# Performance work log

Measured on AMD Instinct MI355X. Metric: run time of the kernel, lower is better.

## Reference

```python
import jax, jax.numpy as jnp
import numpy as np

N, D, H, E = 32768, 1024, 1024, 4


def setup_inputs() -> dict:
    key = jax.random.key(0)
    ks = jax.random.split(key, 10)
    s = 0.02  # xavier-ish init scale for stability
    return {
        "features": jax.random.normal(ks[0], (N, D), dtype=jnp.float32),
        "symbol_ids": jax.random.randint(ks[1], (N,), 0, E, dtype=jnp.int32),
        "W1": jax.random.normal(ks[2], (E, D, H), dtype=jnp.float32) * s,
        "b1": jax.random.normal(ks[3], (E, H), dtype=jnp.float32) * s,
        "W2": jax.random.normal(ks[4], (E, H, H), dtype=jnp.float32) * s,
        "b2": jax.random.normal(ks[5], (E, H), dtype=jnp.float32) * s,
        "W3": jax.random.normal(ks[6], (E, H, 1), dtype=jnp.float32) * s,
        "b3": jax.random.normal(ks[7], (E, 1), dtype=jnp.float32) * s,
        "slope": jax.random.normal(ks[8], (E,), dtype=jnp.float32),
        "intercept": jax.random.normal(ks[9], (E,), dtype=jnp.float32),
    }


def reference(features, symbol_ids, W1, b1, W2, b2, W3, b3, slope, intercept):
    # Run every atom through every expert MLP (E is tiny), then select by symbol.
    # h1: [E, N, H]
    h = jax.nn.relu(jnp.einsum("nd,edh->enh", features, W1) + b1[:, None, :])
    h = jax.nn.relu(jnp.einsum("enh,ehk->enk", h, W2) + b2[:, None, :])
    y = (jnp.einsum("enk,eko->eno", h, W3) + b3[:, None, :])[..., 0]  # [E, N]
    per_atom = slope[:, None] * y + intercept[:, None]                # [E, N]
    sel = symbol_ids[None, :] == jnp.arange(E, dtype=symbol_ids.dtype)[:, None]
    atomic_energies = jnp.sum(jnp.where(sel, per_atom, 0.0), axis=0)  # [N]
    image_energy = jnp.sum(atomic_energies)                           # scalar
    return image_energy
```

## Files before the change

kernel.cpp:

```cpp
#include <hip/hip_runtime.h>
#include <hip/hip_bf16.h>
#include <stdint.h>

#define NATOMS 32768
#define DDIM   1024
#define HDIM   1024
#define ENUM   4
#define MCAP   (NATOMS + ENUM * 128)
#define MTILES 260

typedef unsigned short u16;
typedef unsigned char  u8;
typedef __attribute__((ext_vector_type(8)))  int   i32x8;
typedef __attribute__((ext_vector_type(16))) float f32x16;

static const size_t XP_OFF   = 0;
static const size_t H1_OFF   = XP_OFF  + (size_t)MCAP * 1024;
static const size_t W1T_OFF  = H1_OFF  + (size_t)MCAP * 1024;
static const size_t W2T_OFF  = W1T_OFF + (size_t)ENUM * 1024 * 1024;
static const size_t PERM_OFF = W2T_OFF + (size_t)ENUM * 1024 * 1024;
static const size_t META_OFF = PERM_OFF + (size_t)MCAP * 4;

__device__ __forceinline__ u8 f2fp8(float x) {
    int w = __builtin_amdgcn_cvt_pk_fp8_f32(x, x, 0, false);
    return (u8)(w & 0xFF);
}

__global__ void k_count(const int* __restrict__ sym, int* __restrict__ meta) {
    __shared__ int cnt[4];
    int t = threadIdx.x;
    if (t < 4) cnt[t] = 0;
    __syncthreads();
    int n = blockIdx.x * 256 + t;
    int lane = t & 63;
    int e = sym[n];
#pragma unroll
    for (int j = 0; j < ENUM; ++j) {
        unsigned long long mask = __ballot(e == j);
        if (mask) {
            int leader = __ffsll((long long)mask) - 1;
            if (lane == leader) atomicAdd(&cnt[j], __popcll(mask));
        }
    }
    __syncthreads();
    if (t < 4) meta[256 + blockIdx.x * 4 + t] = cnt[t];
}

__global__ void k_offsets(int* __restrict__ meta, const float* __restrict__ slope,
                          const float* __restrict__ b3, const float* __restrict__ inter,
                          float* __restrict__ out) {
    __shared__ int tot[4];
    int t = threadIdx.x;
    if (t < 4) {
        int s = 0;
#pragma unroll 8
        for (int b = 0; b < 128; ++b) s += meta[256 + b * 4 + t];
        tot[t] = s;
    }
    __syncthreads();
    if (t == 0) {
        int off = 0;
        float c = 0.f;
        for (int e = 0; e < 4; ++e) {
            int cnt = tot[e];
            meta[e * 16]     = cnt;
            meta[128 + e]    = off;
            meta[64 + e*16]  = off;
            c += (float)cnt * (slope[e] * b3[e] + inter[e]);
            off += (cnt + 127) & ~127;
        }
        meta[132] = off;
        out[0] = c;
    }
}

__global__ void k_scatter(const int* __restrict__ sym, int* __restrict__ meta,
                          int* __restrict__ perm) {
    int n = blockIdx.x * 256 + threadIdx.x;
    int lane = threadIdx.x & 63;
    int e = sym[n];
#pragma unroll
    for (int j = 0; j < ENUM; ++j) {
        unsigned long long mask = __ballot(e == j);
        if (mask) {
            int leader = __ffsll((long long)mask) - 1;
            int base = 0;
            if (lane == leader)
                base = atomicAdd(&meta[64 + j * 16], __popcll(mask));
            base = __shfl(base, leader, 64);
            if (e == j) {
                int rank = __popcll(mask & ((1ull << lane) - 1ull));
                perm[base + rank] = n;
            }
        }
    }
}

__global__ void k_convx(const float* __restrict__ F, const int* __restrict__ perm,
                        const int* __restrict__ meta, u8* __restrict__ Xp) {
    int g = blockIdx.x * 256 + threadIdx.x;
    int slot = g >> 7, c = g & 127;
    const int* offs = meta + 128;
    int e = (slot >= offs[1]) + (slot >= offs[2]) + (slot >= offs[3]);
    bool valid = slot < offs[e] + meta[e * 16];
    uint2 v;
    if (!valid) {
        v.x = 0u; v.y = 0u;
    } else {
        int src = perm[slot];
        const float* fp = F + (size_t)src * 1024 + c * 8;
        int w0 = 0, w1 = 0;
        w0 = __builtin_amdgcn_cvt_pk_fp8_f32(fp[0], fp[1], w0, false);
        w0 = __builtin_amdgcn_cvt_pk_fp8_f32(fp[2], fp[3], w0, true);
        w1 = __builtin_amdgcn_cvt_pk_fp8_f32(fp[4], fp[5], w1, false);
        w1 = __builtin_amdgcn_cvt_pk_fp8_f32(fp[6], fp[7], w1, true);
        v.x = (unsigned)w0; v.y = (unsigned)w1;
    }
    *(uint2*)(void*)(Xp + (size_t)g * 8) = v;
}

__global__ void k_transw(const float* __restrict__ W1, u8* __restrict__ W1T,
                         const float* __restrict__ W2, u8* __restrict__ W2T) {
    __shared__ u8 tile[64][65];
    const float* W  = blockIdx.z ? W2  : W1;
    u8*          WT = blockIdx.z ? W2T : W1T;
    int e  = blockIdx.y;
    int tn = blockIdx.x & 15;
    int tk = blockIdx.x >> 4;
    const float* Wp = W  + (size_t)e * 1024 * 1024;
    u8*         WTp = WT + (size_t)e * 1024 * 1024;
    int c = threadIdx.x & 63, r0 = threadIdx.x >> 6;
#pragma unroll
    for (int i = 0; i < 16; ++i) {
        int r = r0 + i * 4;
        tile[r][c] = f2fp8(32.0f * Wp[(size_t)(tk * 64 + r) * 1024 + tn * 64 + c]);
    }
    __syncthreads();
#pragma unroll
    for (int i = 0; i < 16; ++i) {
        int r = r0 + i * 4;
        WTp[(size_t)(tn * 64 + r) * 1024 + tk * 64 + c] = tile[c][r];
    }
}

template <bool FUSE>
__global__ __launch_bounds__(256, 4)
void k_gemm(const u8* __restrict__ A, const u8* __restrict__ BT,
            const float* __restrict__ bias, u8* __restrict__ C,
            const int* __restrict__ meta, const float* __restrict__ W3,
            const float* __restrict__ slope, float* __restrict__ out) {
    __shared__ u8 As[128 * 128];
    __shared__ u8 Bs[128 * 128];
    const int* offs = meta + 128;

    const int flat = blockIdx.y * 8 + blockIdx.x;
    const int mt = (flat >> 6) * 8 + (flat & 7);
    const int nt = (flat & 63) >> 3;
    if (mt >= MTILES) return;
    const int m0 = mt * 128, n0 = nt * 128;
    int e = (m0 >= offs[1]) + (m0 >= offs[2]) + (m0 >= offs[3]);

    const int t = threadIdx.x;
    const int w = t >> 6, lane = t & 63;
    const int l31 = lane & 31, khalf = lane >> 5;
    const int wm = w & 1, wn = w >> 1;

    const u8* Ag = A + (size_t)m0 * 1024;
    const u8* Bg = BT + (size_t)e * 1024 * 1024 + (size_t)n0 * 1024;

    const int srow   = t >> 3;
    const int gchunk = (t & 7) ^ (srow & 7);

    f32x16 acc[2][2] = {};

    for (int kt = 0; kt < 1024 / 128; ++kt) {
        const int kb = kt * 128;
#pragma unroll
        for (int i = 0; i < 4; ++i) {
            int row = i * 32 + srow;
            __builtin_amdgcn_global_load_lds(
                (const void*)(Ag + (size_t)row * 1024 + kb + gchunk * 16),
                (void*)(As + i * 4096 + w * 1024), 16, 0, 0);
        }
#pragma unroll
        for (int i = 0; i < 4; ++i) {
            int row = i * 32 + srow;
            __builtin_amdgcn_global_load_lds(
                (const void*)(Bg + (size_t)row * 1024 + kb + gchunk * 16),
                (void*)(Bs + i * 4096 + w * 1024), 16, 0, 0);
        }
        __syncthreads();

#pragma unroll
        for (int kk = 0; kk < 2; ++kk) {
            const int c0 = 4 * kk + 2 * khalf;
            i32x8 a[2], b[2];
#pragma unroll
            for (int mi = 0; mi < 2; ++mi) {
                int m = wm * 64 + mi * 32 + l31;
                const u8* base = As + m * 128;
                int lo = ((c0 ^ (m & 7)) << 4);
                uint4 q0 = *(const uint4*)(const void*)(base + lo);
                uint4 q1 = *(const uint4*)(const void*)(base + (lo ^ 16));
                union { uint4 q[2]; i32x8 v; } u;
                u.q[0] = q0; u.q[1] = q1;
                a[mi] = u.v;
            }
#pragma unroll
            for (int ni = 0; ni < 2; ++ni) {
                int n = wn * 64 + ni * 32 + l31;
                const u8* base = Bs + n * 128;
                int lo = ((c0 ^ (n & 7)) << 4);
                uint4 q0 = *(const uint4*)(const void*)(base + lo);
                uint4 q1 = *(const uint4*)(const void*)(base + (lo ^ 16));
                union { uint4 q[2]; i32x8 v; } u;
                u.q[0] = q0; u.q[1] = q1;
                b[ni] = u.v;
            }
#pragma unroll
            for (int mi = 0; mi < 2; ++mi)
#pragma unroll
                for (int ni = 0; ni < 2; ++ni)
                    acc[mi][ni] = __builtin_amdgcn_mfma_scale_f32_32x32x64_f8f6f4(
                        a[mi], b[ni], acc[mi][ni],
                        0, 0,
                        0, 0x7F7F7F7F,
                        0, 0x7A7A7A7A);
        }
        __syncthreads();
    }

    if (!FUSE) {
#pragma unroll
        for (int ni = 0; ni < 2; ++ni) {
            int col = n0 + wn * 64 + ni * 32 + l31;
            float bv = bias[e * 1024 + col];
#pragma unroll
            for (int mi = 0; mi < 2; ++mi) {
                int rowb = m0 + wm * 64 + mi * 32 + 4 * khalf;
#pragma unroll
                for (int reg = 0; reg < 16; ++reg) {
                    int rowg = rowb + (reg & 3) + 8 * (reg >> 2);
                    float v = acc[mi][ni][reg] + bv;
                    v = v > 0.f ? v : 0.f;
                    C[(size_t)rowg * 1024 + col] = f2fp8(v);
                }
            }
        }
    } else {
        const int segEnd = offs[e] + meta[e * 16];
        const float se = slope[e];
        float psum = 0.f;
#pragma unroll
        for (int ni = 0; ni < 2; ++ni) {
            int col = n0 + wn * 64 + ni * 32 + l31;
            float bv  = bias[e * 1024 + col];
            float w3s = W3[e * 1024 + col] * se;
#pragma unroll
            for (int mi = 0; mi < 2; ++mi) {
                int rowb = m0 + wm * 64 + mi * 32 + 4 * khalf;
#pragma unroll
                for (int reg = 0; reg < 16; ++reg) {
                    int rowg = rowb + (reg & 3) + 8 * (reg >> 2);
                    float v = acc[mi][ni][reg] + bv;
                    v = v > 0.f ? v : 0.f;
                    psum += (rowg < segEnd) ? v * w3s : 0.f;
                }
            }
        }
#pragma unroll
        for (int o = 32; o; o >>= 1) psum += __shfl_xor(psum, o, 64);
        float* red = (float*)As;
        if (lane == 0) red[w] = psum;
        __syncthreads();
        if (t == 0) atomicAdd(out, red[0] + red[1] + red[2] + red[3]);
    }
}

extern "C" void kernel_launch(void* const* d_in, const int* in_sizes, int n_in,
                              void* d_out, int out_size, void* d_ws, size_t ws_size,
                              hipStream_t stream) {
    const float* features = (const float*)d_in[0];
    const int*   sym      = (const int*)d_in[1];
    const float* W1       = (const float*)d_in[2];
    const float* b1       = (const float*)d_in[3];
    const float* W2       = (const float*)d_in[4];
    const float* b2       = (const float*)d_in[5];
    const float* W3       = (const float*)d_in[6];
    const float* b3       = (const float*)d_in[7];
    const float* slope    = (const float*)d_in[8];
    const float* inter    = (const float*)d_in[9];
    float* out = (float*)d_out;

    char* ws  = (char*)d_ws;
    u8*  Xp   = (u8*)(ws + XP_OFF);
    u8*  H1b  = (u8*)(ws + H1_OFF);
    u8*  W1T  = (u8*)(ws + W1T_OFF);
    u8*  W2T  = (u8*)(ws + W2T_OFF);
    int* perm = (int*)(ws + PERM_OFF);
    int* meta = (int*)(ws + META_OFF);

    k_count<<<NATOMS / 256, 256, 0, stream>>>(sym, meta);
    k_offsets<<<1, 256, 0, stream>>>(meta, slope, b3, inter, out);
    k_scatter<<<NATOMS / 256, 256, 0, stream>>>(sym, meta, perm);
    k_convx<<<(MCAP * 128) / 256, 256, 0, stream>>>(features, perm, meta, Xp);
    k_transw<<<dim3(256, 4, 2), 256, 0, stream>>>(W1, W1T, W2, W2T);
    k_gemm<false><<<dim3(8, 264), 256, 0, stream>>>(Xp, W1T, b1, H1b, meta,
                                                    nullptr, nullptr, nullptr);
    k_gemm<true><<<dim3(8, 264), 256, 0, stream>>>(H1b, W2T, b2, nullptr, meta,
                                                   W3, slope, out);
}
```

Measured before the change: 349.3 us.

## Use 256x256 GEMM tiles with double-buffered LDS prefetch and 8 waves

```diff
diff --git a/kernel.cpp b/kernel.cpp
--- a/kernel.cpp
+++ b/kernel.cpp
@@ -6,8 +6,8 @@
 #define DDIM   1024
 #define HDIM   1024
 #define ENUM   4
-#define MCAP   (NATOMS + ENUM * 128)
-#define MTILES 260
+#define MCAP   33792
+#define MT256  132
 
 typedef unsigned short u16;
 typedef unsigned char  u8;
@@ -67,7 +67,7 @@
             meta[128 + e]    = off;
             meta[64 + e*16]  = off;
             c += (float)cnt * (slope[e] * b3[e] + inter[e]);
-            off += (cnt + 127) & ~127;
+            off += (cnt + 255) & ~255;
         }
         meta[132] = off;
         out[0] = c;
@@ -144,91 +144,113 @@
 }
 
 template <bool FUSE>
-__global__ __launch_bounds__(256, 4)
+__global__ __launch_bounds__(512, 2)
 void k_gemm(const u8* __restrict__ A, const u8* __restrict__ BT,
             const float* __restrict__ bias, u8* __restrict__ C,
             const int* __restrict__ meta, const float* __restrict__ W3,
             const float* __restrict__ slope, float* __restrict__ out) {
-    __shared__ u8 As[128 * 128];
-    __shared__ u8 Bs[128 * 128];
+    __shared__ u8 As[2][32768];
+    __shared__ u8 Bs[2][32768];
     const int* offs = meta + 128;
 
     const int flat = blockIdx.y * 8 + blockIdx.x;
-    const int mt = (flat >> 6) * 8 + (flat & 7);
-    const int nt = (flat & 63) >> 3;
-    if (mt >= MTILES) return;
-    const int m0 = mt * 128, n0 = nt * 128;
-    int e = (m0 >= offs[1]) + (m0 >= offs[2]) + (m0 >= offs[3]);
+    const int wgid = (flat & 7) * 66 + (flat >> 3);
+    const int mt = wgid >> 2;
+    const int nt = wgid & 3;
+    const int m0 = mt * 256, n0 = nt * 256;
+    if (m0 >= meta[132]) return;
+    const int e = (m0 >= offs[1]) + (m0 >= offs[2]) + (m0 >= offs[3]);
 
     const int t = threadIdx.x;
     const int w = t >> 6, lane = t & 63;
     const int l31 = lane & 31, khalf = lane >> 5;
     const int wm = w & 1, wn = w >> 1;
 
-    const u8* Ag = A + (size_t)m0 * 1024;
+    const u8* Ag = A  + (size_t)m0 * 1024;
     const u8* Bg = BT + (size_t)e * 1024 * 1024 + (size_t)n0 * 1024;
 
-    const int srow   = t >> 3;
-    const int gchunk = (t & 7) ^ (srow & 7);
-
-    f32x16 acc[2][2] = {};
-
-    for (int kt = 0; kt < 1024 / 128; ++kt) {
-        const int kb = kt * 128;
-#pragma unroll
-        for (int i = 0; i < 4; ++i) {
-            int row = i * 32 + srow;
-            __builtin_amdgcn_global_load_lds(
-                (const void*)(Ag + (size_t)row * 1024 + kb + gchunk * 16),
-                (void*)(As + i * 4096 + w * 1024), 16, 0, 0);
-        }
-#pragma unroll
-        for (int i = 0; i < 4; ++i) {
-            int row = i * 32 + srow;
-            __builtin_amdgcn_global_load_lds(
-                (const void*)(Bg + (size_t)row * 1024 + kb + gchunk * 16),
-                (void*)(Bs + i * 4096 + w * 1024), 16, 0, 0);
-        }
-        __syncthreads();
-
-#pragma unroll
-        for (int kk = 0; kk < 2; ++kk) {
-            const int c0 = 4 * kk + 2 * khalf;
-            i32x8 a[2], b[2];
-#pragma unroll
-            for (int mi = 0; mi < 2; ++mi) {
-                int m = wm * 64 + mi * 32 + l31;
-                const u8* base = As + m * 128;
+    const int srow = t >> 3;
+    const int gcol = ((t & 7) ^ (srow & 7)) * 16;
+
+    f32x16 acc[4][2] = {};
+
+#define STAGE(buf, kt)                                                          \
+    do {                                                                        \
+        const size_t kb = (size_t)(kt) * 128;                                   \
+        _Pragma("unroll")                                                       \
+        for (int i = 0; i < 4; ++i) {                                           \
+            __builtin_amdgcn_global_load_lds(                                   \
+                (const void*)(Ag + (size_t)(i * 64 + srow) * 1024 + kb + gcol), \
+                (void*)(&As[buf][i * 8192 + w * 1024]), 16, 0, 0);              \
+            __builtin_amdgcn_global_load_lds(                                   \
+                (const void*)(Bg + (size_t)(i * 64 + srow) * 1024 + kb + gcol), \
+                (void*)(&Bs[buf][i * 8192 + w * 1024]), 16, 0, 0);              \
+        }                                                                       \
+    } while (0)
+
+    STAGE(0, 0);
+
+#pragma unroll 2
+    for (int kt = 0; kt < 8; ++kt) {
+        const int cur = kt & 1;
+        asm volatile("" ::: "memory");
+        __builtin_amdgcn_s_barrier();
+        asm volatile("" ::: "memory");
+        if (kt < 7) {
+            STAGE(cur ^ 1, kt + 1);
+            asm volatile("s_waitcnt vmcnt(8)" ::: "memory");
+        } else {
+            asm volatile("s_waitcnt vmcnt(0)" ::: "memory");
+        }
+        __builtin_amdgcn_s_barrier();
+        asm volatile("" ::: "memory");
+
+        const u8* Ab = &As[cur][0];
+        const u8* Bb = &Bs[cur][0];
+
+        i32x8 b[2][2];
+#pragma unroll
+        for (int ni = 0; ni < 2; ++ni)
+#pragma unroll
+            for (int ks = 0; ks < 2; ++ks) {
+                int n = wn * 64 + ni * 32 + l31;
+                int c0 = 4 * ks + 2 * khalf;
+                const u8* base = Bb + n * 128;
+                int lo = ((c0 ^ (n & 7)) << 4);
+                union { uint4 q[2]; i32x8 v; } u;
+                u.q[0] = *(const uint4*)(const void*)(base + lo);
+                u.q[1] = *(const uint4*)(const void*)(base + (lo ^ 16));
+                b[ni][ks] = u.v;
+            }
+
+#pragma unroll
+        for (int mi = 0; mi < 4; ++mi) {
+            i32x8 a[2];
+#pragma unroll
+            for (int ks = 0; ks < 2; ++ks) {
+                int m = wm * 128 + mi * 32 + l31;
+                int c0 = 4 * ks + 2 * khalf;
+                const u8* base = Ab + m * 128;
                 int lo = ((c0 ^ (m & 7)) << 4);
-                uint4 q0 = *(const uint4*)(const void*)(base + lo);
-                uint4 q1 = *(const uint4*)(const void*)(base + (lo ^ 16));
                 union { uint4 q[2]; i32x8 v; } u;
-                u.q[0] = q0; u.q[1] = q1;
-                a[mi] = u.v;
-            }
-#pragma unroll
-            for (int ni = 0; ni < 2; ++ni) {
-                int n = wn * 64 + ni * 32 + l31;
-                const u8* base = Bs + n * 128;
-                int lo = ((c0 ^ (n & 7)) << 4);
-                uint4 q0 = *(const uint4*)(const void*)(base + lo);
-                uint4 q1 = *(const uint4*)(const void*)(base + (lo ^ 16));
-                union { uint4 q[2]; i32x8 v; } u;
-                u.q[0] = q0; u.q[1] = q1;
-                b[ni] = u.v;
-            }
-#pragma unroll
-            for (int mi = 0; mi < 2; ++mi)
-#pragma unroll
-                for (int ni = 0; ni < 2; ++ni)
+                u.q[0] = *(const uint4*)(const void*)(base + lo);
+                u.q[1] = *(const uint4*)(const void*)(base + (lo ^ 16));
+                a[ks] = u.v;
+            }
+            __builtin_amdgcn_s_setprio(1);
+#pragma unroll
+            for (int ni = 0; ni < 2; ++ni)
+#pragma unroll
+                for (int ks = 0; ks < 2; ++ks)
                     acc[mi][ni] = __builtin_amdgcn_mfma_scale_f32_32x32x64_f8f6f4(
-                        a[mi], b[ni], acc[mi][ni],
+                        a[ks], b[ni][ks], acc[mi][ni],
                         0, 0,
                         0, 0x7F7F7F7F,
                         0, 0x7A7A7A7A);
-        }
-        __syncthreads();
-    }
+            __builtin_amdgcn_s_setprio(0);
+        }
+    }
+#undef STAGE
 
     if (!FUSE) {
 #pragma unroll
@@ -236,8 +258,8 @@
             int col = n0 + wn * 64 + ni * 32 + l31;
             float bv = bias[e * 1024 + col];
 #pragma unroll
-            for (int mi = 0; mi < 2; ++mi) {
-                int rowb = m0 + wm * 64 + mi * 32 + 4 * khalf;
+            for (int mi = 0; mi < 4; ++mi) {
+                int rowb = m0 + wm * 128 + mi * 32 + 4 * khalf;
 #pragma unroll
                 for (int reg = 0; reg < 16; ++reg) {
                     int rowg = rowb + (reg & 3) + 8 * (reg >> 2);
@@ -257,8 +279,8 @@
             float bv  = bias[e * 1024 + col];
             float w3s = W3[e * 1024 + col] * se;
 #pragma unroll
-            for (int mi = 0; mi < 2; ++mi) {
-                int rowb = m0 + wm * 64 + mi * 32 + 4 * khalf;
+            for (int mi = 0; mi < 4; ++mi) {
+                int rowb = m0 + wm * 128 + mi * 32 + 4 * khalf;
 #pragma unroll
                 for (int reg = 0; reg < 16; ++reg) {
                     int rowg = rowb + (reg & 3) + 8 * (reg >> 2);
@@ -270,10 +292,16 @@
         }
 #pragma unroll
         for (int o = 32; o; o >>= 1) psum += __shfl_xor(psum, o, 64);
+        __syncthreads();
         float* red = (float*)As;
         if (lane == 0) red[w] = psum;
         __syncthreads();
-        if (t == 0) atomicAdd(out, red[0] + red[1] + red[2] + red[3]);
+        if (t == 0) {
+            float s = 0.f;
+#pragma unroll
+            for (int i = 0; i < 8; ++i) s += red[i];
+            atomicAdd(out, s);
+        }
     }
 }
 
@@ -305,8 +333,8 @@
     k_scatter<<<NATOMS / 256, 256, 0, stream>>>(sym, meta, perm);
     k_convx<<<(MCAP * 128) / 256, 256, 0, stream>>>(features, perm, meta, Xp);
     k_transw<<<dim3(256, 4, 2), 256, 0, stream>>>(W1, W1T, W2, W2T);
-    k_gemm<false><<<dim3(8, 264), 256, 0, stream>>>(Xp, W1T, b1, H1b, meta,
-                                                    nullptr, nullptr, nullptr);
-    k_gemm<true><<<dim3(8, 264), 256, 0, stream>>>(H1b, W2T, b2, nullptr, meta,
-                                                   W3, slope, out);
-}
+    k_gemm<false><<<dim3(8, 66), 512, 0, stream>>>(Xp, W1T, b1, H1b, meta,
+                                                   nullptr, nullptr, nullptr);
+    k_gemm<true><<<dim3(8, 66), 512, 0, stream>>>(H1b, W2T, b2, nullptr, meta,
+                                                  W3, slope, out);
+}
```

Measured after the change: 377.3 us. +8.0%, slower.

## Enlarge GEMM M-tile to 256 rows and remap workgroups for weight reuse

Applied to the files above, without the earlier changes.

```diff
diff --git a/kernel.cpp b/kernel.cpp
--- a/kernel.cpp
+++ b/kernel.cpp
@@ -6,8 +6,7 @@
 #define DDIM   1024
 #define HDIM   1024
 #define ENUM   4
-#define MCAP   (NATOMS + ENUM * 128)
-#define MTILES 260
+#define MCAP   33792
 
 typedef unsigned short u16;
 typedef unsigned char  u8;
@@ -67,7 +66,7 @@
             meta[128 + e]    = off;
             meta[64 + e*16]  = off;
             c += (float)cnt * (slope[e] * b3[e] + inter[e]);
-            off += (cnt + 127) & ~127;
+            off += (cnt + 255) & ~255;
         }
         meta[132] = off;
         out[0] = c;
@@ -144,49 +143,48 @@
 }
 
 template <bool FUSE>
-__global__ __launch_bounds__(256, 4)
+__global__ __launch_bounds__(256, 2)
 void k_gemm(const u8* __restrict__ A, const u8* __restrict__ BT,
             const float* __restrict__ bias, u8* __restrict__ C,
             const int* __restrict__ meta, const float* __restrict__ W3,
             const float* __restrict__ slope, float* __restrict__ out) {
-    __shared__ u8 As[128 * 128];
+    __shared__ u8 As[256 * 128];
     __shared__ u8 Bs[128 * 128];
     const int* offs = meta + 128;
 
     const int flat = blockIdx.y * 8 + blockIdx.x;
-    const int mt = (flat >> 6) * 8 + (flat & 7);
-    const int nt = (flat & 63) >> 3;
-    if (mt >= MTILES) return;
-    const int m0 = mt * 128, n0 = nt * 128;
-    int e = (m0 >= offs[1]) + (m0 >= offs[2]) + (m0 >= offs[3]);
+    const int wgid = (flat & 7) * 132 + (flat >> 3);
+    const int mt = wgid >> 3;
+    const int nt = wgid & 7;
+    const int m0 = mt * 256, n0 = nt * 128;
+    if (m0 >= meta[132]) return;
+    const int e = (m0 >= offs[1]) + (m0 >= offs[2]) + (m0 >= offs[3]);
 
     const int t = threadIdx.x;
     const int w = t >> 6, lane = t & 63;
     const int l31 = lane & 31, khalf = lane >> 5;
     const int wm = w & 1, wn = w >> 1;
 
-    const u8* Ag = A + (size_t)m0 * 1024;
+    const u8* Ag = A  + (size_t)m0 * 1024;
     const u8* Bg = BT + (size_t)e * 1024 * 1024 + (size_t)n0 * 1024;
 
     const int srow   = t >> 3;
-    const int gchunk = (t & 7) ^ (srow & 7);
-
-    f32x16 acc[2][2] = {};
+    const int gcol   = ((t & 7) ^ (srow & 7)) * 16;
+
+    f32x16 acc[4][2] = {};
 
     for (int kt = 0; kt < 1024 / 128; ++kt) {
         const int kb = kt * 128;
 #pragma unroll
+        for (int i = 0; i < 8; ++i) {
+            __builtin_amdgcn_global_load_lds(
+                (const void*)(Ag + (size_t)(i * 32 + srow) * 1024 + kb + gcol),
+                (void*)(As + i * 4096 + w * 1024), 16, 0, 0);
+        }
+#pragma unroll
         for (int i = 0; i < 4; ++i) {
-            int row = i * 32 + srow;
             __builtin_amdgcn_global_load_lds(
-                (const void*)(Ag + (size_t)row * 1024 + kb + gchunk * 16),
-                (void*)(As + i * 4096 + w * 1024), 16, 0, 0);
-        }
-#pragma unroll
-        for (int i = 0; i < 4; ++i) {
-            int row = i * 32 + srow;
-            __builtin_amdgcn_global_load_lds(
-                (const void*)(Bg + (size_t)row * 1024 + kb + gchunk * 16),
+                (const void*)(Bg + (size_t)(i * 32 + srow) * 1024 + kb + gcol),
                 (void*)(Bs + i * 4096 + w * 1024), 16, 0, 0);
         }
         __syncthreads();
@@ -194,38 +192,34 @@
 #pragma unroll
         for (int kk = 0; kk < 2; ++kk) {
             const int c0 = 4 * kk + 2 * khalf;
-            i32x8 a[2], b[2];
-#pragma unroll
-            for (int mi = 0; mi < 2; ++mi) {
-                int m = wm * 64 + mi * 32 + l31;
-                const u8* base = As + m * 128;
-                int lo = ((c0 ^ (m & 7)) << 4);
-                uint4 q0 = *(const uint4*)(const void*)(base + lo);
-                uint4 q1 = *(const uint4*)(const void*)(base + (lo ^ 16));
-                union { uint4 q[2]; i32x8 v; } u;
-                u.q[0] = q0; u.q[1] = q1;
-                a[mi] = u.v;
-            }
+            i32x8 b[2];
 #pragma unroll
             for (int ni = 0; ni < 2; ++ni) {
                 int n = wn * 64 + ni * 32 + l31;
                 const u8* base = Bs + n * 128;
                 int lo = ((c0 ^ (n & 7)) << 4);
-                uint4 q0 = *(const uint4*)(const void*)(base + lo);
-                uint4 q1 = *(const uint4*)(const void*)(base + (lo ^ 16));
                 union { uint4 q[2]; i32x8 v; } u;
-                u.q[0] = q0; u.q[1] = q1;
+                u.q[0] = *(const uint4*)(const void*)(base + lo);
+                u.q[1] = *(const uint4*)(const void*)(base + (lo ^ 16));
                 b[ni] = u.v;
             }
 #pragma unroll
-            for (int mi = 0; mi < 2; ++mi)
+            for (int mi = 0; mi < 4; ++mi) {
+                int m = wm * 128 + mi * 32 + l31;
+                const u8* base = As + m * 128;
+                int lo = ((c0 ^ (m & 7)) << 4);
+                union { uint4 q[2]; i32x8 v; } u;
+                u.q[0] = *(const uint4*)(const void*)(base + lo);
+                u.q[1] = *(const uint4*)(const void*)(base + (lo ^ 16));
+                i32x8 a = u.v;
 #pragma unroll
                 for (int ni = 0; ni < 2; ++ni)
                     acc[mi][ni] = __builtin_amdgcn_mfma_scale_f32_32x32x64_f8f6f4(
-                        a[mi], b[ni], acc[mi][ni],
+                        a, b[ni], acc[mi][ni],
                         0, 0,
                         0, 0x7F7F7F7F,
                         0, 0x7A7A7A7A);
+            }
         }
         __syncthreads();
     }
@@ -236,8 +230,8 @@
             int col = n0 + wn * 64 + ni * 32 + l31;
             float bv = bias[e * 1024 + col];
 #pragma unroll
-            for (int mi = 0; mi < 2; ++mi) {
-                int rowb = m0 + wm * 64 + mi * 32 + 4 * khalf;
+            for (int mi = 0; mi < 4; ++mi) {
+                int rowb = m0 + wm * 128 + mi * 32 + 4 * khalf;
 #pragma unroll
                 for (int reg = 0; reg < 16; ++reg) {
                     int rowg = rowb + (reg & 3) + 8 * (reg >> 2);
@@ -257,8 +251,8 @@
             float bv  = bias[e * 1024 + col];
             float w3s = W3[e * 1024 + col] * se;
 #pragma unroll
-            for (int mi = 0; mi < 2; ++mi) {
-                int rowb = m0 + wm * 64 + mi * 32 + 4 * khalf;
+            for (int mi = 0; mi < 4; ++mi) {
+                int rowb = m0 + wm * 128 + mi * 32 + 4 * khalf;
 #pragma unroll
                 for (int reg = 0; reg < 16; ++reg) {
                     int rowg = rowb + (reg & 3) + 8 * (reg >> 2);
@@ -305,8 +299,8 @@
     k_scatter<<<NATOMS / 256, 256, 0, stream>>>(sym, meta, perm);
     k_convx<<<(MCAP * 128) / 256, 256, 0, stream>>>(features, perm, meta, Xp);
     k_transw<<<dim3(256, 4, 2), 256, 0, stream>>>(W1, W1T, W2, W2T);
-    k_gemm<false><<<dim3(8, 264), 256, 0, stream>>>(Xp, W1T, b1, H1b, meta,
+    k_gemm<false><<<dim3(8, 132), 256, 0, stream>>>(Xp, W1T, b1, H1b, meta,
                                                     nullptr, nullptr, nullptr);
-    k_gemm<true><<<dim3(8, 264), 256, 0, stream>>>(H1b, W2T, b2, nullptr, meta,
+    k_gemm<true><<<dim3(8, 132), 256, 0, stream>>>(H1b, W2T, b2, nullptr, meta,
                                                    W3, slope, out);
 }
```

Result: no change. 347.4 us (-0.5%).
